# Optimization experiments

Hardware: AMD Instinct MI355X
Metric: run time of the kernel (lower is better)

## Reference

```python
import jax, jax.numpy as jnp
import numpy as np

MARGIN = 0.3
BIG = 9999999.0


def setup_inputs() -> dict:
    key = jax.random.key(0)
    k1, k2 = jax.random.split(key)
    emb = jax.random.normal(k1, (4096, 2048), dtype=jnp.float32)
    label = jax.random.randint(k2, (4096,), 0, 64, dtype=jnp.int64 if jax.config.jax_enable_x64 else jnp.int32)
    return {"emb": emb, "label": label}


def euclidean_dist(x, y):
    xx = jnp.sum(x * x, axis=1, keepdims=True)          # [m,1]
    yy = jnp.sum(y * y, axis=1, keepdims=True).T        # [1,n]
    dist = xx + yy - 2.0 * (x @ y.T)                    # [m,n]
    return jnp.sqrt(jnp.clip(dist, 1e-12, None))


def reference(emb, label):
    mat_dist = euclidean_dist(emb, emb)                 # [N,N]
    mat_sim = (label[:, None] == label[None, :]).astype(mat_dist.dtype)
    # batch-hard mining: top-1 of masked sorts == masked max / min reductions
    dist_ap = jnp.max(mat_dist - BIG * (1.0 - mat_sim), axis=1)  # hardest positive
    dist_an = jnp.min(mat_dist + BIG * mat_sim, axis=1)          # hardest negative
    # MarginRankingLoss(dist_an, dist_ap, y=1): mean(relu(margin - (dist_an - dist_ap)))
    loss = jnp.mean(jax.nn.relu(MARGIN - (dist_an - dist_ap)))
    prec = jnp.mean((dist_an > dist_ap).astype(jnp.float32))
    return (loss, prec)
```

## Files before the change

kernel.cpp:

```cpp
#include <hip/hip_runtime.h>

#define N_ROWS 4096
#define D_K    2048
#define BP   128
#define NPAN (N_ROWS / BP)
#define NTRI (NPAN * (NPAN + 1) / 2)
#define BK   32
#define NT   (D_K / BK)
#define MARGIN 0.3f

typedef unsigned short u16;
typedef __attribute__((ext_vector_type(8))) short bf16x8;
typedef __attribute__((ext_vector_type(4))) float f32x4;

__device__ __forceinline__ void stage16(const u16* src, u16* dst) {
    __builtin_amdgcn_global_load_lds((const __attribute__((address_space(1))) unsigned int*)src,
                                     (__attribute__((address_space(3))) unsigned int*)dst, 16, 0, 0);
}

__device__ __forceinline__ u16 f2bf(float f) {
    unsigned u = __float_as_uint(f);
    u += 0x7fffu + ((u >> 16) & 1u);
    return (u16)(u >> 16);
}

__global__ __launch_bounds__(256) void prep_kernel(
    const float* __restrict__ emb, u16* __restrict__ embB,
    float* __restrict__ xx, unsigned* __restrict__ ap2, unsigned* __restrict__ an2)
{
    const int row = blockIdx.x;
    const int t = threadIdx.x;
    const float4* src = (const float4*)(emb + (size_t)row * D_K);
    ushort4* dst = (ushort4*)(embB + (size_t)row * D_K);
    float s = 0.f;
#pragma unroll
    for (int i = 0; i < 2; ++i) {
        float4 v = src[t + i * 256];
        s = fmaf(v.x, v.x, s);
        s = fmaf(v.y, v.y, s);
        s = fmaf(v.z, v.z, s);
        s = fmaf(v.w, v.w, s);
        ushort4 o;
        o.x = f2bf(v.x); o.y = f2bf(v.y); o.z = f2bf(v.z); o.w = f2bf(v.w);
        dst[t + i * 256] = o;
    }
#pragma unroll
    for (int off = 32; off >= 1; off >>= 1) s += __shfl_down(s, off, 64);
    __shared__ float red[4];
    if ((t & 63) == 0) red[t >> 6] = s;
    __syncthreads();
    if (t == 0) {
        xx[row] = red[0] + red[1] + red[2] + red[3];
        ap2[row] = 0u;
        an2[row] = 0x7f7fffffu;
    }
}

#define LDv(p) (*(const bf16x8*)(p))

__global__ __launch_bounds__(256) void gram_tri_kernel(
    const u16* __restrict__ embB, const float* __restrict__ xx,
    const int* __restrict__ lab, unsigned* __restrict__ ap2, unsigned* __restrict__ an2)
{
    __shared__ u16 As[BP * BK];
    __shared__ u16 Bs[BP * BK];
    __shared__ int labR[BP], labC[BP];
    __shared__ float xxR[BP], xxC[BP];

    const int tid = threadIdx.x;

    const int bid = blockIdx.x;
    const int p = (bid & 7) * (NTRI / 8) + (bid >> 3);
    int I = 0, rem = p;
    while (rem >= NPAN - I) { rem -= NPAN - I; ++I; }
    const int J = I + rem;
    const int row0 = I * BP, col0 = J * BP;
    const bool diag = (I == J);

    const int csw = ((tid & 3) ^ ((tid >> 3) & 3)) * 8;
    const int srow = tid >> 2;
    const u16* gA0 = embB + (size_t)(row0 + srow) * D_K + csw;
    const u16* gA1 = embB + (size_t)(row0 + 64 + srow) * D_K + csw;
    const u16* gB0 = embB + (size_t)(col0 + srow) * D_K + csw;
    const u16* gB1 = embB + (size_t)(col0 + 64 + srow) * D_K + csw;
    u16* lA = As + tid * 8;
    u16* lB = Bs + tid * 8;

    const int l = tid & 63, w = tid >> 6;
    const int wr = w >> 1, wc = w & 1;
    const int fr = l & 15, fkb = l >> 4;
    const int kx = (fkb ^ ((fr >> 1) & 3)) * 16;
    const char* AB = (const char*)As;
    const char* BB = (const char*)Bs;
    const int aOff = wr * 4096 + fr * 64;
    const int bOff = wc * 4096 + fr * 64;

    f32x4 acc[4][4];
#pragma unroll
    for (int m = 0; m < 4; ++m)
#pragma unroll
        for (int n = 0; n < 4; ++n) acc[m][n] = (f32x4){0.f, 0.f, 0.f, 0.f};

    for (int kt = 0; kt < NT; ++kt) {
        const int ko = kt * BK;
        stage16(gA0 + ko, lA); stage16(gA1 + ko, lA + 2048);
        stage16(gB0 + ko, lB); stage16(gB1 + ko, lB + 2048);
        __syncthreads();
        bf16x8 aq[4], bq[4];
#pragma unroll
        for (int m = 0; m < 4; ++m) aq[m] = LDv(AB + aOff + m * 1024 + kx);
#pragma unroll
        for (int n = 0; n < 4; ++n) bq[n] = LDv(BB + bOff + n * 1024 + kx);
#pragma unroll
        for (int m = 0; m < 4; ++m)
#pragma unroll
            for (int n = 0; n < 4; ++n)
                acc[m][n] = __builtin_amdgcn_mfma_f32_16x16x32_bf16(aq[m], bq[n], acc[m][n], 0, 0, 0);
        __syncthreads();
    }

    if (tid < BP)      { labR[tid] = lab[row0 + tid]; xxR[tid] = xx[row0 + tid]; }
    else               { int u2 = tid - BP; labC[u2] = lab[col0 + u2]; xxC[u2] = xx[col0 + u2]; }
    __syncthreads();

    const int rgrp = l >> 4;

#pragma unroll
    for (int m = 0; m < 4; ++m) {
#pragma unroll
        for (int r = 0; r < 4; ++r) {
            const int il = wr * 64 + m * 16 + rgrp * 4 + r;
            const int li = labR[il];
            const float xi = xxR[il];
            float apv = 0.f, anv = __FLT_MAX__;
#pragma unroll
            for (int n = 0; n < 4; ++n) {
                const int jl = wc * 64 + n * 16 + fr;
                float d2 = xi + xxC[jl] - 2.f * acc[m][n][r];
                d2 = fmaxf(d2, 1e-12f);
                const bool same = (labC[jl] == li);
                apv = same ? fmaxf(apv, d2) : apv;
                anv = same ? anv : fminf(anv, d2);
            }
#pragma unroll
            for (int off = 1; off < 16; off <<= 1) {
                apv = fmaxf(apv, __shfl_xor(apv, off, 64));
                anv = fminf(anv, __shfl_xor(anv, off, 64));
            }
            if (fr == 0) {
                atomicMax(&ap2[row0 + il], __float_as_uint(apv));
                atomicMin(&an2[row0 + il], __float_as_uint(anv));
            }
        }
    }

    if (!diag) {
#pragma unroll
        for (int n = 0; n < 4; ++n) {
            const int jl = wc * 64 + n * 16 + fr;
            const int lj = labC[jl];
            const float xj = xxC[jl];
            float apv = 0.f, anv = __FLT_MAX__;
#pragma unroll
            for (int m = 0; m < 4; ++m) {
#pragma unroll
                for (int r = 0; r < 4; ++r) {
                    const int il = wr * 64 + m * 16 + rgrp * 4 + r;
                    float d2 = xj + xxR[il] - 2.f * acc[m][n][r];
                    d2 = fmaxf(d2, 1e-12f);
                    const bool same = (labR[il] == lj);
                    apv = same ? fmaxf(apv, d2) : apv;
                    anv = same ? anv : fminf(anv, d2);
                }
            }
            apv = fmaxf(apv, __shfl_xor(apv, 16, 64));
            anv = fminf(anv, __shfl_xor(anv, 16, 64));
            apv = fmaxf(apv, __shfl_xor(apv, 32, 64));
            anv = fminf(anv, __shfl_xor(anv, 32, 64));
            if (rgrp == 0) {
                atomicMax(&ap2[col0 + jl], __float_as_uint(apv));
                atomicMin(&an2[col0 + jl], __float_as_uint(anv));
            }
        }
    }
}

__global__ __launch_bounds__(256) void finalize_kernel(
    const unsigned* __restrict__ ap2, const unsigned* __restrict__ an2, float* __restrict__ out)
{
    const int t = threadIdx.x;
    float ls = 0.f, ps = 0.f;
    for (int i = t; i < N_ROWS; i += 256) {
        const float ap = sqrtf(__uint_as_float(ap2[i]));
        const float an = sqrtf(__uint_as_float(an2[i]));
        ls += fmaxf(MARGIN - an + ap, 0.f);
        ps += (an > ap) ? 1.f : 0.f;
    }
#pragma unroll
    for (int off = 32; off >= 1; off >>= 1) {
        ls += __shfl_down(ls, off, 64);
        ps += __shfl_down(ps, off, 64);
    }
    __shared__ float rl[4], rp[4];
    if ((t & 63) == 0) { rl[t >> 6] = ls; rp[t >> 6] = ps; }
    __syncthreads();
    if (t == 0) {
        out[0] = (rl[0] + rl[1] + rl[2] + rl[3]) * (1.f / N_ROWS);
        out[1] = (rp[0] + rp[1] + rp[2] + rp[3]) * (1.f / N_ROWS);
    }
}

extern "C" void kernel_launch(void* const* d_in, const int* in_sizes, int n_in,
                              void* d_out, int out_size, void* d_ws, size_t ws_size,
                              hipStream_t stream)
{
    const float* emb = (const float*)d_in[0];
    const int* lab = (const int*)d_in[1];
    float* out = (float*)d_out;

    char* ws = (char*)d_ws;
    u16* embB   = (u16*)ws;
    float* xx   = (float*)(ws + (size_t)N_ROWS * D_K * 2);
    unsigned* ap2 = (unsigned*)(ws + (size_t)N_ROWS * D_K * 2 + N_ROWS * 4);
    unsigned* an2 = (unsigned*)(ws + (size_t)N_ROWS * D_K * 2 + 2 * (size_t)N_ROWS * 4);

    prep_kernel<<<N_ROWS, 256, 0, stream>>>(emb, embB, xx, ap2, an2);
    gram_tri_kernel<<<NTRI, 256, 0, stream>>>(embB, xx, lab, ap2, an2);
    finalize_kernel<<<1, 256, 0, stream>>>(ap2, an2, out);
}
```

Baseline: 74.87 us.

## Triple-buffer LDS tiles with prefetch two k-steps ahead and vmcnt waits

Replaces the single-buffered K loop, which had two barriers per step, with a three-stage LDS ring. Global-to-LDS loads for tile k+2 are issued before the MFMAs for tile k run. Each step then waits with an explicit vmcnt and a single raw s_barrier. The goal is to hide global load latency behind compute. The cost is triple the LDS footprint, which may lower occupancy, plus fragile hand-written waitcnt and barrier correctness.

```diff
diff --git a/kernel.cpp b/kernel.cpp
--- a/kernel.cpp
+++ b/kernel.cpp
@@ -57,13 +57,41 @@
 }
 
 #define LDv(p) (*(const bf16x8*)(p))
+#define BARRIER()  __builtin_amdgcn_s_barrier()
+#define VMW_(n)    asm volatile("s_waitcnt vmcnt(" #n ")" ::: "memory")
+#define VMW(n)     VMW_(n)
+
+#define STAGE32(B3_, KTE_) do {                        \
+    stage16(gA0 + (KTE_), lA + (B3_) * 4096);          \
+    stage16(gA1 + (KTE_), lA + (B3_) * 4096 + 2048);   \
+    stage16(gB0 + (KTE_), lB + (B3_) * 4096);          \
+    stage16(gB1 + (KTE_), lB + (B3_) * 4096 + 2048);   \
+} while (0)
+
+#define KT32(B_, T_)                                                                  \
+  {                                                                                   \
+    const bool ok = ((T_) + 2 < NT);                                                  \
+    if (ok) { STAGE32(((B_) + 2) % 3, ((T_) + 2) * BK); }                             \
+    bf16x8 aq[4], bq[4];                                                              \
+    _Pragma("unroll")                                                                 \
+    for (int n = 0; n < 4; ++n) bq[n] = LDv(BB + (B_) * 8192 + bOff + n * 1024 + kx); \
+    _Pragma("unroll")                                                                 \
+    for (int m = 0; m < 4; ++m) aq[m] = LDv(AB + (B_) * 8192 + aOff + m * 1024 + kx); \
+    _Pragma("unroll")                                                                 \
+    for (int m = 0; m < 4; ++m)                                                       \
+        _Pragma("unroll")                                                             \
+        for (int n = 0; n < 4; ++n)                                                   \
+            acc[m][n] = __builtin_amdgcn_mfma_f32_16x16x32_bf16(aq[m], bq[n], acc[m][n], 0, 0, 0); \
+    if (ok) { VMW(4); } else { VMW(0); }                                              \
+    BARRIER();                                                                        \
+  }
 
 __global__ __launch_bounds__(256) void gram_tri_kernel(
     const u16* __restrict__ embB, const float* __restrict__ xx,
     const int* __restrict__ lab, unsigned* __restrict__ ap2, unsigned* __restrict__ an2)
 {
-    __shared__ u16 As[BP * BK];
-    __shared__ u16 Bs[BP * BK];
+    __shared__ u16 As[3 * BP * BK];
+    __shared__ u16 Bs[3 * BP * BK];
     __shared__ int labR[BP], labC[BP];
     __shared__ float xxR[BP], xxC[BP];
 
@@ -101,23 +129,18 @@
 #pragma unroll
         for (int n = 0; n < 4; ++n) acc[m][n] = (f32x4){0.f, 0.f, 0.f, 0.f};
 
-    for (int kt = 0; kt < NT; ++kt) {
-        const int ko = kt * BK;
-        stage16(gA0 + ko, lA); stage16(gA1 + ko, lA + 2048);
-        stage16(gB0 + ko, lB); stage16(gB1 + ko, lB + 2048);
-        __syncthreads();
-        bf16x8 aq[4], bq[4];
-#pragma unroll
-        for (int m = 0; m < 4; ++m) aq[m] = LDv(AB + aOff + m * 1024 + kx);
-#pragma unroll
-        for (int n = 0; n < 4; ++n) bq[n] = LDv(BB + bOff + n * 1024 + kx);
-#pragma unroll
-        for (int m = 0; m < 4; ++m)
-#pragma unroll
-            for (int n = 0; n < 4; ++n)
-                acc[m][n] = __builtin_amdgcn_mfma_f32_16x16x32_bf16(aq[m], bq[n], acc[m][n], 0, 0, 0);
-        __syncthreads();
-    }
+    STAGE32(0, 0);
+    STAGE32(1, BK);
+    VMW(4);
+    BARRIER();
+
+    for (int ii = 0; ii < 21; ++ii) {
+        const int t3 = 3 * ii;
+        KT32(0, t3)
+        KT32(1, t3 + 1)
+        KT32(2, t3 + 2)
+    }
+    KT32(0, 63)
 
     if (tid < BP)      { labR[tid] = lab[row0 + tid]; xxR[tid] = xx[row0 + tid]; }
     else               { int u2 = tid - BP; labC[u2] = lab[col0 + u2]; xxC[u2] = xx[col0 + u2]; }
```

After: 100.4 us. +34.1%, slower.

## Double-buffer LDS tiles with BK=64 and prefetch the next k-tile

Applied to the files above, without the earlier changes.

The k-tile depth of the Gram kernel doubles from 32 to 64, and shared memory now holds two A/B buffers. The global-to-LDS copy of the next tile is issued before the MFMA work on the current tile, so each k-step needs one barrier instead of two. The LDS XOR swizzle is widened to 8 chunks to match the 128-byte row stride. The aim is to hide global load latency and halve barrier count, at the cost of 64 KB of LDS per block, which may reduce occupancy.

```diff
diff --git a/kernel.cpp b/kernel.cpp
--- a/kernel.cpp
+++ b/kernel.cpp
@@ -5,7 +5,7 @@
 #define BP   128
 #define NPAN (N_ROWS / BP)
 #define NTRI (NPAN * (NPAN + 1) / 2)
-#define BK   32
+#define BK   64
 #define NT   (D_K / BK)
 #define MARGIN 0.3f
 
@@ -58,12 +58,47 @@
 
 #define LDv(p) (*(const bf16x8*)(p))
 
+#define STAGE64(B_, KTE_) do {                                       \
+    stage16(gA + 0 * r32 + (KTE_), lA + (B_) * 8192 +    0);         \
+    stage16(gA + 1 * r32 + (KTE_), lA + (B_) * 8192 + 2048);         \
+    stage16(gA + 2 * r32 + (KTE_), lA + (B_) * 8192 + 4096);         \
+    stage16(gA + 3 * r32 + (KTE_), lA + (B_) * 8192 + 6144);         \
+    stage16(gB + 0 * r32 + (KTE_), lB + (B_) * 8192 +    0);         \
+    stage16(gB + 1 * r32 + (KTE_), lB + (B_) * 8192 + 2048);         \
+    stage16(gB + 2 * r32 + (KTE_), lB + (B_) * 8192 + 4096);         \
+    stage16(gB + 3 * r32 + (KTE_), lB + (B_) * 8192 + 6144);         \
+} while (0)
+
+#define KT64(B_, NB_, T_)                                                              \
+  {                                                                                    \
+    if ((T_) + 1 < NT) { STAGE64(NB_, ((T_) + 1) * BK); }                              \
+    bf16x8 aq[4][2], bq[4][2];                                                         \
+    _Pragma("unroll")                                                                  \
+    for (int m = 0; m < 4; ++m) {                                                      \
+        aq[m][0] = LDv(AB + (B_) * 16384 + aOff + m * 2048 + kx0);                     \
+        aq[m][1] = LDv(AB + (B_) * 16384 + aOff + m * 2048 + kx1);                     \
+    }                                                                                  \
+    _Pragma("unroll")                                                                  \
+    for (int n = 0; n < 4; ++n) {                                                      \
+        bq[n][0] = LDv(BB + (B_) * 16384 + bOff + n * 2048 + kx0);                     \
+        bq[n][1] = LDv(BB + (B_) * 16384 + bOff + n * 2048 + kx1);                     \
+    }                                                                                  \
+    _Pragma("unroll")                                                                  \
+    for (int ks = 0; ks < 2; ++ks)                                                     \
+        _Pragma("unroll")                                                              \
+        for (int m = 0; m < 4; ++m)                                                    \
+            _Pragma("unroll")                                                          \
+            for (int n = 0; n < 4; ++n)                                                \
+                acc[m][n] = __builtin_amdgcn_mfma_f32_16x16x32_bf16(aq[m][ks], bq[n][ks], acc[m][n], 0, 0, 0); \
+    __syncthreads();                                                                   \
+  }
+
 __global__ __launch_bounds__(256) void gram_tri_kernel(
     const u16* __restrict__ embB, const float* __restrict__ xx,
     const int* __restrict__ lab, unsigned* __restrict__ ap2, unsigned* __restrict__ an2)
 {
-    __shared__ u16 As[BP * BK];
-    __shared__ u16 Bs[BP * BK];
+    __shared__ u16 As[2 * BP * BK];
+    __shared__ u16 Bs[2 * BP * BK];
     __shared__ int labR[BP], labC[BP];
     __shared__ float xxR[BP], xxC[BP];
 
@@ -77,23 +112,23 @@
     const int row0 = I * BP, col0 = J * BP;
     const bool diag = (I == J);
 
-    const int csw = ((tid & 3) ^ ((tid >> 3) & 3)) * 8;
-    const int srow = tid >> 2;
-    const u16* gA0 = embB + (size_t)(row0 + srow) * D_K + csw;
-    const u16* gA1 = embB + (size_t)(row0 + 64 + srow) * D_K + csw;
-    const u16* gB0 = embB + (size_t)(col0 + srow) * D_K + csw;
-    const u16* gB1 = embB + (size_t)(col0 + 64 + srow) * D_K + csw;
+    const int csw = ((tid & 7) ^ ((tid >> 3) & 7)) * 8;
+    const int srow = tid >> 3;
+    const u16* gA = embB + (size_t)(row0 + srow) * D_K + csw;
+    const u16* gB = embB + (size_t)(col0 + srow) * D_K + csw;
+    const size_t r32 = (size_t)32 * D_K;
     u16* lA = As + tid * 8;
     u16* lB = Bs + tid * 8;
 
     const int l = tid & 63, w = tid >> 6;
     const int wr = w >> 1, wc = w & 1;
     const int fr = l & 15, fkb = l >> 4;
-    const int kx = (fkb ^ ((fr >> 1) & 3)) * 16;
+    const int kx0 = (fkb ^ (fr & 7)) * 16;
+    const int kx1 = kx0 ^ 64;
     const char* AB = (const char*)As;
     const char* BB = (const char*)Bs;
-    const int aOff = wr * 4096 + fr * 64;
-    const int bOff = wc * 4096 + fr * 64;
+    const int aOff = wr * 8192 + fr * 128;
+    const int bOff = wc * 8192 + fr * 128;
 
     f32x4 acc[4][4];
 #pragma unroll
@@ -101,22 +136,13 @@
 #pragma unroll
         for (int n = 0; n < 4; ++n) acc[m][n] = (f32x4){0.f, 0.f, 0.f, 0.f};
 
-    for (int kt = 0; kt < NT; ++kt) {
-        const int ko = kt * BK;
-        stage16(gA0 + ko, lA); stage16(gA1 + ko, lA + 2048);
-        stage16(gB0 + ko, lB); stage16(gB1 + ko, lB + 2048);
-        __syncthreads();
-        bf16x8 aq[4], bq[4];
-#pragma unroll
-        for (int m = 0; m < 4; ++m) aq[m] = LDv(AB + aOff + m * 1024 + kx);
-#pragma unroll
-        for (int n = 0; n < 4; ++n) bq[n] = LDv(BB + bOff + n * 1024 + kx);
-#pragma unroll
-        for (int m = 0; m < 4; ++m)
-#pragma unroll
-            for (int n = 0; n < 4; ++n)
-                acc[m][n] = __builtin_amdgcn_mfma_f32_16x16x32_bf16(aq[m], bq[n], acc[m][n], 0, 0, 0);
-        __syncthreads();
+    STAGE64(0, 0);
+    __syncthreads();
+
+    for (int ii = 0; ii < NT / 2; ++ii) {
+        const int t2 = 2 * ii;
+        KT64(0, 1, t2)
+        KT64(1, 0, t2 + 1)
     }
 
     if (tid < BP)      { labR[tid] = lab[row0 + tid]; xxR[tid] = xx[row0 + tid]; }
```

Result: slower. 101.3 us (+35.3%).

## Use 128x64 rectangular tiles over the upper triangle to double block count

Applied to the files above, without the earlier changes.

Replaces the 128x128 triangular tiling (528 blocks) with 128x64 tiles covering the upper triangle at 64-column granularity (1056 blocks). Each block does half the MFMA work and always runs the column-side reduction, because the diagonal 128x128 panel is now covered by two 64-wide tiles. The intent is better load balance and more resident waves across the CUs. The cost is lower data reuse per tile, more atomic traffic, and some redundant computation in the diagonal tiles.

```diff
diff --git a/kernel.cpp b/kernel.cpp
--- a/kernel.cpp
+++ b/kernel.cpp
@@ -2,9 +2,10 @@
 
 #define N_ROWS 4096
 #define D_K    2048
-#define BP   128
-#define NPAN (N_ROWS / BP)
-#define NTRI (NPAN * (NPAN + 1) / 2)
+#define BPR  128
+#define BPC  64
+#define NPC  (N_ROWS / BPC)
+#define NTILE 1056
 #define BK   32
 #define NT   (D_K / BK)
 #define MARGIN 0.3f
@@ -62,27 +63,25 @@
     const u16* __restrict__ embB, const float* __restrict__ xx,
     const int* __restrict__ lab, unsigned* __restrict__ ap2, unsigned* __restrict__ an2)
 {
-    __shared__ u16 As[BP * BK];
-    __shared__ u16 Bs[BP * BK];
-    __shared__ int labR[BP], labC[BP];
-    __shared__ float xxR[BP], xxC[BP];
+    __shared__ u16 As[BPR * BK];
+    __shared__ u16 Bs[BPC * BK];
+    __shared__ int labR[BPR], labC[BPC];
+    __shared__ float xxR[BPR], xxC[BPC];
 
     const int tid = threadIdx.x;
 
     const int bid = blockIdx.x;
-    const int p = (bid & 7) * (NTRI / 8) + (bid >> 3);
+    const int p = (bid & 7) * (NTILE / 8) + (bid >> 3);
     int I = 0, rem = p;
-    while (rem >= NPAN - I) { rem -= NPAN - I; ++I; }
-    const int J = I + rem;
-    const int row0 = I * BP, col0 = J * BP;
-    const bool diag = (I == J);
+    while (rem >= NPC - 2 * I) { rem -= NPC - 2 * I; ++I; }
+    const int Jc = 2 * I + rem;
+    const int row0 = I * BPR, col0 = Jc * BPC;
 
     const int csw = ((tid & 3) ^ ((tid >> 3) & 3)) * 8;
     const int srow = tid >> 2;
     const u16* gA0 = embB + (size_t)(row0 + srow) * D_K + csw;
     const u16* gA1 = embB + (size_t)(row0 + 64 + srow) * D_K + csw;
-    const u16* gB0 = embB + (size_t)(col0 + srow) * D_K + csw;
-    const u16* gB1 = embB + (size_t)(col0 + 64 + srow) * D_K + csw;
+    const u16* gB  = embB + (size_t)(col0 + srow) * D_K + csw;
     u16* lA = As + tid * 8;
     u16* lB = Bs + tid * 8;
 
@@ -93,34 +92,34 @@
     const char* AB = (const char*)As;
     const char* BB = (const char*)Bs;
     const int aOff = wr * 4096 + fr * 64;
-    const int bOff = wc * 4096 + fr * 64;
-
-    f32x4 acc[4][4];
+    const int bOff = wc * 2048 + fr * 64;
+
+    f32x4 acc[4][2];
 #pragma unroll
     for (int m = 0; m < 4; ++m)
 #pragma unroll
-        for (int n = 0; n < 4; ++n) acc[m][n] = (f32x4){0.f, 0.f, 0.f, 0.f};
+        for (int n = 0; n < 2; ++n) acc[m][n] = (f32x4){0.f, 0.f, 0.f, 0.f};
 
     for (int kt = 0; kt < NT; ++kt) {
         const int ko = kt * BK;
         stage16(gA0 + ko, lA); stage16(gA1 + ko, lA + 2048);
-        stage16(gB0 + ko, lB); stage16(gB1 + ko, lB + 2048);
+        stage16(gB + ko, lB);
         __syncthreads();
-        bf16x8 aq[4], bq[4];
+        bf16x8 aq[4], bq[2];
 #pragma unroll
         for (int m = 0; m < 4; ++m) aq[m] = LDv(AB + aOff + m * 1024 + kx);
 #pragma unroll
-        for (int n = 0; n < 4; ++n) bq[n] = LDv(BB + bOff + n * 1024 + kx);
+        for (int n = 0; n < 2; ++n) bq[n] = LDv(BB + bOff + n * 1024 + kx);
 #pragma unroll
         for (int m = 0; m < 4; ++m)
 #pragma unroll
-            for (int n = 0; n < 4; ++n)
+            for (int n = 0; n < 2; ++n)
                 acc[m][n] = __builtin_amdgcn_mfma_f32_16x16x32_bf16(aq[m], bq[n], acc[m][n], 0, 0, 0);
         __syncthreads();
     }
 
-    if (tid < BP)      { labR[tid] = lab[row0 + tid]; xxR[tid] = xx[row0 + tid]; }
-    else               { int u2 = tid - BP; labC[u2] = lab[col0 + u2]; xxC[u2] = xx[col0 + u2]; }
+    if (tid < BPR)            { labR[tid] = lab[row0 + tid]; xxR[tid] = xx[row0 + tid]; }
+    else if (tid < BPR + BPC) { int u2 = tid - BPR; labC[u2] = lab[col0 + u2]; xxC[u2] = xx[col0 + u2]; }
     __syncthreads();
 
     const int rgrp = l >> 4;
@@ -134,8 +133,8 @@
             const float xi = xxR[il];
             float apv = 0.f, anv = __FLT_MAX__;
 #pragma unroll
-            for (int n = 0; n < 4; ++n) {
-                const int jl = wc * 64 + n * 16 + fr;
+            for (int n = 0; n < 2; ++n) {
+                const int jl = wc * 32 + n * 16 + fr;
                 float d2 = xi + xxC[jl] - 2.f * acc[m][n][r];
                 d2 = fmaxf(d2, 1e-12f);
                 const bool same = (labC[jl] == li);
@@ -154,33 +153,31 @@
         }
     }
 
-    if (!diag) {
-#pragma unroll
-        for (int n = 0; n < 4; ++n) {
-            const int jl = wc * 64 + n * 16 + fr;
-            const int lj = labC[jl];
-            const float xj = xxC[jl];
-            float apv = 0.f, anv = __FLT_MAX__;
-#pragma unroll
-            for (int m = 0; m < 4; ++m) {
-#pragma unroll
-                for (int r = 0; r < 4; ++r) {
-                    const int il = wr * 64 + m * 16 + rgrp * 4 + r;
-                    float d2 = xj + xxR[il] - 2.f * acc[m][n][r];
-                    d2 = fmaxf(d2, 1e-12f);
-                    const bool same = (labR[il] == lj);
-                    apv = same ? fmaxf(apv, d2) : apv;
-                    anv = same ? anv : fminf(anv, d2);
-                }
-            }
-            apv = fmaxf(apv, __shfl_xor(apv, 16, 64));
-            anv = fminf(anv, __shfl_xor(anv, 16, 64));
-            apv = fmaxf(apv, __shfl_xor(apv, 32, 64));
-            anv = fminf(anv, __shfl_xor(anv, 32, 64));
-            if (rgrp == 0) {
-                atomicMax(&ap2[col0 + jl], __float_as_uint(apv));
-                atomicMin(&an2[col0 + jl], __float_as_uint(anv));
-            }
+#pragma unroll
+    for (int n = 0; n < 2; ++n) {
+        const int jl = wc * 32 + n * 16 + fr;
+        const int lj = labC[jl];
+        const float xj = xxC[jl];
+        float apv = 0.f, anv = __FLT_MAX__;
+#pragma unroll
+        for (int m = 0; m < 4; ++m) {
+#pragma unroll
+            for (int r = 0; r < 4; ++r) {
+                const int il = wr * 64 + m * 16 + rgrp * 4 + r;
+                float d2 = xj + xxR[il] - 2.f * acc[m][n][r];
+                d2 = fmaxf(d2, 1e-12f);
+                const bool same = (labR[il] == lj);
+                apv = same ? fmaxf(apv, d2) : apv;
+                anv = same ? anv : fminf(anv, d2);
+            }
+        }
+        apv = fmaxf(apv, __shfl_xor(apv, 16, 64));
+        anv = fminf(anv, __shfl_xor(anv, 16, 64));
+        apv = fmaxf(apv, __shfl_xor(apv, 32, 64));
+        anv = fminf(anv, __shfl_xor(anv, 32, 64));
+        if (rgrp == 0) {
+            atomicMax(&ap2[col0 + jl], __float_as_uint(apv));
+            atomicMin(&an2[col0 + jl], __float_as_uint(anv));
         }
     }
 }
@@ -225,6 +222,6 @@
     unsigned* an2 = (unsigned*)(ws + (size_t)N_ROWS * D_K * 2 + 2 * (size_t)N_ROWS * 4);
 
     prep_kernel<<<N_ROWS, 256, 0, stream>>>(emb, embB, xx, ap2, an2);
-    gram_tri_kernel<<<NTRI, 256, 0, stream>>>(embB, xx, lab, ap2, an2);
+    gram_tri_kernel<<<NTILE, 256, 0, stream>>>(embB, xx, lab, ap2, an2);
     finalize_kernel<<<1, 256, 0, stream>>>(ap2, an2, out);
 }
```

Result: slower. 97.91 us (+30.8%).
